# Performance work log

Measured on AMD Instinct MI355X. Metric: run time of the kernel, lower is better.

## Reference

```python
import jax, jax.numpy as jnp
import numpy as np

NW, K, C, H = 4096, 32, 256, 8
HD = C // H
POS_BND = 25            # int(0.8 * patch_size * dilation**0.5) = int(0.8*32)
RPE_NUM = 2 * POS_BND + 1  # 51; table has 3*51 = 153 rows


def setup_inputs() -> dict:
    key = jax.random.key(0)
    ks = jax.random.split(key, 10)
    s = 0.02
    return {
        "data": jax.random.normal(ks[0], (NW * K, C), jnp.float32),
        "mask": jax.random.normal(ks[1], (NW, K, K), jnp.float32),
        "rel_pos": jax.random.randint(ks[2], (NW, K, K, 3), -POS_BND, POS_BND + 1, jnp.int32),
        "qkv_w": jax.random.normal(ks[3], (C, 3 * C), jnp.float32) * s,
        "qkv_b": jnp.zeros((3 * C,), jnp.float32),
        "proj_w": jax.random.normal(ks[4], (C, C), jnp.float32) * s,
        "proj_b": jnp.zeros((C,), jnp.float32),
        "rpe_table": jax.random.normal(ks[5], (3 * RPE_NUM, H), jnp.float32) * s,
        "ln1_g": jnp.ones((C,), jnp.float32),
        "ln1_b": jnp.zeros((C,), jnp.float32),
        "ln2_g": jnp.ones((C,), jnp.float32),
        "ln2_b": jnp.zeros((C,), jnp.float32),
        "fc1_w": jax.random.normal(ks[6], (C, 4 * C), jnp.float32) * s,
        "fc1_b": jnp.zeros((4 * C,), jnp.float32),
        "fc2_w": jax.random.normal(ks[7], (4 * C, C), jnp.float32) * s,
        "fc2_b": jnp.zeros((C,), jnp.float32),
    }


def _ln(x, g, b):
    m = jnp.mean(x, axis=-1, keepdims=True)
    v = jnp.var(x, axis=-1, keepdims=True)
    return (x - m) * jax.lax.rsqrt(v + 1e-5) * g + b


def reference(data, mask, rel_pos, qkv_w, qkv_b, proj_w, proj_b, rpe_table,
              ln1_g, ln1_b, ln2_g, ln2_b, fc1_w, fc1_b, fc2_w, fc2_b):
    scale = float(HD) ** -0.5
    # pre-norm attention branch
    x = _ln(data, ln1_g, ln1_b)
    qkv = (x @ qkv_w + qkv_b).reshape(NW, K, 3, H, HD)
    q, k, v = qkv[:, :, 0], qkv[:, :, 1], qkv[:, :, 2]   # [NW,K,H,HD]
    attn = jnp.einsum('wqhd,wkhd->whqk', q * scale, k)   # [NW,H,K,K]
    # RPE: clamp xyz offsets, offset each axis into its table band, gather+sum
    idx = jnp.clip(rel_pos, -POS_BND, POS_BND) + POS_BND + jnp.arange(3) * RPE_NUM
    bias = rpe_table[idx].sum(axis=3)                    # [NW,K,K,H]
    attn = attn + bias.transpose(0, 3, 1, 2) + mask[:, None]
    attn = jax.nn.softmax(attn, axis=-1)
    out = jnp.einsum('whqk,wkhd->wqhd', attn, v).reshape(NW * K, C)
    data = data + (out @ proj_w + proj_b)
    # pre-norm MLP branch
    h = _ln(data, ln2_g, ln2_b)
    h = jax.nn.gelu(h @ fc1_w + fc1_b) @ fc2_w + fc2_b
    return data + h
```

## Files before the change

### kernel.cpp

```cpp
#include <hip/hip_runtime.h>

#define NWIN 4096
#define KTOK 32
#define CH 256
#define NH 8
#define NTOK (NWIN*KTOK)

typedef unsigned short bf16u;
typedef __attribute__((ext_vector_type(4))) float f32x4;
typedef __attribute__((ext_vector_type(4))) unsigned short u16x4;
typedef __attribute__((ext_vector_type(8))) unsigned short u16x8;
typedef __attribute__((ext_vector_type(8))) __bf16 bf16x8;

__device__ __forceinline__ unsigned short f2bf(float f) {
  unsigned u = __builtin_bit_cast(unsigned, f);
  u += 0x7fffu + ((u >> 16) & 1u);
  return (unsigned short)(u >> 16);
}

__device__ __forceinline__ f32x4 mfma16(bf16x8 a, bf16x8 b, f32x4 c) {
  return __builtin_amdgcn_mfma_f32_16x16x32_bf16(a, b, c, 0, 0, 0);
}

__device__ __forceinline__ void gl16(const void* g, void* l) {
  __builtin_amdgcn_global_load_lds(
      (const __attribute__((address_space(1))) unsigned int*)g,
      (__attribute__((address_space(3))) unsigned int*)l, 16, 0, 0);
}

__device__ __forceinline__ float gelu_f(float x) {
  float u = x + 0.044715f * x * x * x;
  return x * __builtin_amdgcn_rcpf(1.f + __expf(-1.5957691216057308f * u));
}

__global__ __launch_bounds__(256) void wprep_kernel(const float* __restrict__ W,
                                                    bf16u* __restrict__ Wt,
                                                    int Kd, int Nd) {
  int idx = blockIdx.x * 256 + threadIdx.x;
  if (idx >= Kd * Nd) return;
  int k = idx / Nd, n = idx - k * Nd;
  Wt[n * Kd + k] = f2bf(W[idx]);
}

__global__ __launch_bounds__(256) void ln_kernel(const float* __restrict__ x,
                                                 const float* __restrict__ g,
                                                 const float* __restrict__ b,
                                                 bf16u* __restrict__ y) {
  const int row = blockIdx.x * 4 + (threadIdx.x >> 6);
  const int lane = threadIdx.x & 63;
  const size_t base = (size_t)row * CH + lane * 4;
  const f32x4 v = *(const f32x4*)(x + base);
  float s = v[0] + v[1] + v[2] + v[3];
  float q = v[0]*v[0] + v[1]*v[1] + v[2]*v[2] + v[3]*v[3];
  #pragma unroll
  for (int d = 32; d; d >>= 1) { s += __shfl_xor(s, d); q += __shfl_xor(q, d); }
  const float mean = s * (1.f/256.f);
  const float rs = rsqrtf(q * (1.f/256.f) - mean*mean + 1e-5f);
  const f32x4 gv = *(const f32x4*)(g + lane*4);
  const f32x4 bv = *(const f32x4*)(b + lane*4);
  u16x4 o;
  #pragma unroll
  for (int d = 0; d < 4; ++d) o[d] = f2bf((v[d]-mean)*rs*gv[d] + bv[d]);
  *(u16x4*)(y + base) = o;
}

template<int EPI>
__global__ __launch_bounds__(256, 4)
void gemm_kernel(const bf16u* __restrict__ A, const bf16u* __restrict__ Bt,
                 const float* __restrict__ bias, const float* __restrict__ resid,
                 void* __restrict__ out, int M, int N, int K, int nx) {
  __shared__ __align__(16) char lds[32768];
  const int tid = threadIdx.x;
  const int lane = tid & 63;
  const int wv = tid >> 6;
  const int lo = lane & 15, hi = lane >> 4;
  const int nwg = gridDim.x;
  const int cpx = nwg >> 3;
  const int swz = (blockIdx.x & 7) * cpx + (blockIdx.x >> 3);
  const int by = swz / nx, bx = swz - by * nx;
  const int bm = by * 128, bn = bx * 128;
  const int wm = (wv >> 1) * 64, wn = (wv & 1) * 64;

  f32x4 acc[4][4] = {};

  const int srow = tid >> 2;
  const int sk = (tid & 3) * 16;
  const size_t rstep = (size_t)64 * K * 2;
  const char* gA = (const char*)(A + (size_t)(bm + srow) * K) + sk;
  const char* gB = (const char*)(Bt + (size_t)(bn + srow) * K) + sk;

  auto STAGE = [&](int b, int k0) {
    char* As = lds + b * 16384;
    char* Bs = As + 8192;
    const char* ga = gA + k0 * 2;
    const char* gb = gB + k0 * 2;
    gl16(ga,         As + tid*16);
    gl16(ga + rstep, As + 4096 + tid*16);
    gl16(gb,         Bs + tid*16);
    gl16(gb + rstep, Bs + 4096 + tid*16);
  };

  STAGE(0, 0);
  int cur = 0;
  for (int k0 = 0; ; k0 += 32) {
    const bool has_next = (k0 + 32 < K);
    if (has_next) {
      STAGE(cur ^ 1, k0 + 32);
      asm volatile("s_waitcnt vmcnt(4)" ::: "memory");
    } else {
      asm volatile("s_waitcnt vmcnt(0)" ::: "memory");
    }
    __builtin_amdgcn_sched_barrier(0);
    __builtin_amdgcn_s_barrier();
    const char* As = lds + cur * 16384;
    const char* Bs = As + 8192;
    bf16x8 af[4], bfv[4];
    #pragma unroll
    for (int i = 0; i < 4; ++i) {
      af[i]  = *(const bf16x8*)(As + (wm + i*16 + lo)*64 + hi*16);
      bfv[i] = *(const bf16x8*)(Bs + (wn + i*16 + lo)*64 + hi*16);
    }
    #pragma unroll
    for (int i = 0; i < 4; ++i)
      #pragma unroll
      for (int j = 0; j < 4; ++j)
        acc[i][j] = mfma16(af[i], bfv[j], acc[i][j]);
    if (!has_next) break;
    __builtin_amdgcn_s_barrier();
    cur ^= 1;
  }

  __syncthreads();
  float* Ls = (float*)(lds + wv * 4352);
  const int mb = bm + wm, nb = bn + wn;
  const int lrow = lane >> 3;
  const int lcol = (lane & 7) * 8;
  const f32x4 bv0 = *(const f32x4*)(bias + nb + lcol);
  const f32x4 bv1 = *(const f32x4*)(bias + nb + lcol + 4);

  #pragma unroll
  for (int i = 0; i < 4; ++i) {
    #pragma unroll
    for (int j = 0; j < 4; ++j)
      #pragma unroll
      for (int r = 0; r < 4; ++r)
        Ls[(hi*4 + r)*68 + j*16 + lo] = acc[i][j][r];
    #pragma unroll
    for (int p = 0; p < 2; ++p) {
      const int rr = p*8 + lrow;
      const int m = mb + i*16 + rr;
      f32x4 v0 = *(const f32x4*)(Ls + rr*68 + lcol);
      f32x4 v1 = *(const f32x4*)(Ls + rr*68 + lcol + 4);
      v0 += bv0; v1 += bv1;
      if constexpr (EPI == 2) {
        const float* rp = resid + (size_t)m*N + nb + lcol;
        v0 += *(const f32x4*)rp;
        v1 += *(const f32x4*)(rp + 4);
        float* op = (float*)out + (size_t)m*N + nb + lcol;
        *(f32x4*)op = v0;
        *(f32x4*)(op + 4) = v1;
      } else {
        if constexpr (EPI == 1) {
          #pragma unroll
          for (int d = 0; d < 4; ++d) { v0[d] = gelu_f(v0[d]); v1[d] = gelu_f(v1[d]); }
        }
        u16x8 o8;
        #pragma unroll
        for (int d = 0; d < 4; ++d) { o8[d] = f2bf(v0[d]); o8[4+d] = f2bf(v1[d]); }
        *(u16x8*)((bf16u*)out + (size_t)m*N + nb + lcol) = o8;
      }
    }
  }
}

__global__ __launch_bounds__(256, 2)
void attn_kernel(const bf16u* __restrict__ qkv, const float* __restrict__ mask,
                 const int* __restrict__ relp, const float* __restrict__ rpe,
                 bf16u* __restrict__ outp) {
  const int w = blockIdx.x;
  const int tid = threadIdx.x, lane = tid & 63, wv = tid >> 6;
  const int lo = lane & 15, hi = lane >> 4;

  __shared__ __align__(16) bf16u sQK[32*520];
  __shared__ __align__(16) bf16u sV[32][264];
  __shared__ __align__(16) bf16u sP[4][32][44];
  __shared__ float sTabT[8][156];
  __shared__ int sRel[1024];
  __shared__ float sMask[32][33];

  const size_t qbase = (size_t)w * (32*768);
  {
    #pragma unroll
    for (int t = 0; t < 8; ++t) {
      int i = tid + t*256;
      int tok = i >> 6;
      int cb = (i & 63) * 16;
      *(u16x8*)((char*)sQK + tok*1040 + cb) =
          *(const u16x8*)((const char*)(qkv + qbase) + tok*1536 + cb);
    }
    #pragma unroll
    for (int t = 0; t < 4; ++t) {
      int i = tid + t*256;
      int tok = i >> 5, c8 = i & 31;
      *(u16x8*)&sV[tok][c8*8] = *(const u16x8*)(qkv + qbase + tok*768 + 512 + c8*8);
    }
    for (int i = tid; i < 1224; i += 256)
      sTabT[i & 7][i >> 3] = rpe[i];
    #pragma unroll
    for (int t = 0; t < 4; ++t) {
      int i = tid + t*256;
      const int* rp = relp + ((size_t)w*1024 + i)*3;
      int r0 = rp[0], r1 = rp[1], r2 = rp[2];
      r0 = min(max(r0, -25), 25) + 25;
      r1 = min(max(r1, -25), 25) + 76;
      r2 = min(max(r2, -25), 25) + 127;
      sRel[i] = r0 | (r1 << 8) | (r2 << 16);
    }
    #pragma unroll
    for (int d = 0; d < 4; ++d) {
      int i = tid*4 + d;
      sMask[i >> 5][i & 31] = mask[(size_t)w*1024 + i];
    }
  }
  __syncthreads();

  const float scale = 0.17677669529663687f;
  #pragma unroll
  for (int e = 0; e < 2; ++e) {
    const int h = wv*2 + e;
    bf16x8 qf[2], kf[2];
    #pragma unroll
    for (int rf = 0; rf < 2; ++rf) {
      int tok = rf*16 + lo;
      qf[rf] = *(const bf16x8*)((const char*)sQK + tok*1040 + h*64 + hi*16);
      kf[rf] = *(const bf16x8*)((const char*)sQK + tok*1040 + 512 + h*64 + hi*16);
    }
    f32x4 S[2][2] = {};
    #pragma unroll
    for (int rf = 0; rf < 2; ++rf)
      #pragma unroll
      for (int cf = 0; cf < 2; ++cf)
        S[rf][cf] = mfma16(qf[rf], kf[cf], S[rf][cf]);
    #pragma unroll
    for (int rf = 0; rf < 2; ++rf)
      #pragma unroll
      for (int cf = 0; cf < 2; ++cf)
        #pragma unroll
        for (int r = 0; r < 4; ++r) {
          const int qq = rf*16 + hi*4 + r;
          const int kk = cf*16 + lo;
          const int pk = sRel[qq*32 + kk];
          const float bsum = sTabT[h][pk & 255] + sTabT[h][(pk >> 8) & 255]
                           + sTabT[h][(pk >> 16) & 255];
          S[rf][cf][r] = S[rf][cf][r] * scale + bsum + sMask[qq][kk];
        }
    #pragma unroll
    for (int rf = 0; rf < 2; ++rf)
      #pragma unroll
      for (int r = 0; r < 4; ++r) {
        float m0 = fmaxf(S[rf][0][r], S[rf][1][r]);
        #pragma unroll
        for (int d = 1; d < 16; d <<= 1) m0 = fmaxf(m0, __shfl_xor(m0, d));
        const float p0 = __expf(S[rf][0][r] - m0);
        const float p1 = __expf(S[rf][1][r] - m0);
        float ss = p0 + p1;
        #pragma unroll
        for (int d = 1; d < 16; d <<= 1) ss += __shfl_xor(ss, d);
        const float inv = 1.f / ss;
        S[rf][0][r] = p0 * inv;
        S[rf][1][r] = p1 * inv;
      }
    #pragma unroll
    for (int rf = 0; rf < 2; ++rf)
      #pragma unroll
      for (int cf = 0; cf < 2; ++cf)
        #pragma unroll
        for (int r = 0; r < 4; ++r)
          sP[wv][rf*16 + hi*4 + r][cf*16 + lo] = f2bf(S[rf][cf][r]);
    f32x4 O[2][2] = {};
    #pragma unroll
    for (int rf = 0; rf < 2; ++rf) {
      bf16x8 pf;
      *(u16x4*)&pf       = *(const u16x4*)&sP[wv][rf*16 + lo][hi*8];
      *((u16x4*)&pf + 1) = *(const u16x4*)&sP[wv][rf*16 + lo][hi*8 + 4];
      #pragma unroll
      for (int cf = 0; cf < 2; ++cf) {
        bf16x8 vf;
        #pragma unroll
        for (int j = 0; j < 8; ++j)
          ((bf16u*)&vf)[j] = sV[hi*8 + j][h*32 + cf*16 + lo];
        O[rf][cf] = mfma16(pf, vf, O[rf][cf]);
      }
    }
    #pragma unroll
    for (int rf = 0; rf < 2; ++rf)
      #pragma unroll
      for (int cf = 0; cf < 2; ++cf)
        #pragma unroll
        for (int r = 0; r < 4; ++r) {
          const int qq = rf*16 + hi*4 + r;
          outp[(size_t)(w*32 + qq)*256 + h*32 + cf*16 + lo] = f2bf(O[rf][cf][r]);
        }
  }
}

extern "C" void kernel_launch(void* const* d_in, const int* in_sizes, int n_in,
                              void* d_out, int out_size, void* d_ws, size_t ws_size,
                              hipStream_t stream) {
  const float* data   = (const float*)d_in[0];
  const float* mask   = (const float*)d_in[1];
  const int*   relp   = (const int*)d_in[2];
  const float* qkv_w  = (const float*)d_in[3];
  const float* qkv_b  = (const float*)d_in[4];
  const float* proj_w = (const float*)d_in[5];
  const float* proj_b = (const float*)d_in[6];
  const float* rpe    = (const float*)d_in[7];
  const float* ln1_g  = (const float*)d_in[8];
  const float* ln1_b  = (const float*)d_in[9];
  const float* ln2_g  = (const float*)d_in[10];
  const float* ln2_b  = (const float*)d_in[11];
  const float* fc1_w  = (const float*)d_in[12];
  const float* fc1_b  = (const float*)d_in[13];
  const float* fc2_w  = (const float*)d_in[14];
  const float* fc2_b  = (const float*)d_in[15];

  char* ws = (char*)d_ws;
  bf16u* wt_qkv  = (bf16u*)(ws);
  bf16u* wt_proj = (bf16u*)(ws + 393216);
  bf16u* wt_fc1  = (bf16u*)(ws + 524288);
  bf16u* wt_fc2  = (bf16u*)(ws + 1048576);
  bf16u* xbuf    = (bf16u*)(ws + 2097152);
  bf16u* qkvbuf  = (bf16u*)(ws + 2097152 + 67108864);
  float* data2   = (float*)d_out;

  wprep_kernel<<<768, 256, 0, stream>>>(qkv_w, wt_qkv, 256, 768);
  wprep_kernel<<<256, 256, 0, stream>>>(proj_w, wt_proj, 256, 256);
  wprep_kernel<<<1024, 256, 0, stream>>>(fc1_w, wt_fc1, 256, 1024);
  wprep_kernel<<<1024, 256, 0, stream>>>(fc2_w, wt_fc2, 1024, 256);

  ln_kernel<<<32768, 256, 0, stream>>>(data, ln1_g, ln1_b, xbuf);
  gemm_kernel<0><<<6*1024, 256, 0, stream>>>(xbuf, wt_qkv, qkv_b, nullptr,
                                             qkvbuf, NTOK, 768, 256, 6);
  attn_kernel<<<NWIN, 256, 0, stream>>>(qkvbuf, mask, relp, rpe, xbuf);
  gemm_kernel<2><<<2*1024, 256, 0, stream>>>(xbuf, wt_proj, proj_b, data,
                                             data2, NTOK, 256, 256, 2);
  ln_kernel<<<32768, 256, 0, stream>>>(data2, ln2_g, ln2_b, xbuf);
  gemm_kernel<1><<<8*1024, 256, 0, stream>>>(xbuf, wt_fc1, fc1_b, nullptr,
                                             qkvbuf, NTOK, 1024, 256, 8);
  gemm_kernel<2><<<2*1024, 256, 0, stream>>>(qkvbuf, wt_fc2, fc2_b, data2,
                                             d_out, NTOK, 256, 1024, 2);
}
```

Measured before the change: 623.3 us.

## Fuse LayerNorm into GEMM A-loads and triple-buffer the K-loop GEMM

LayerNorm gamma is folded into the transposed bf16 weights, and beta is folded into a precomputed bias (W^T·beta + b). That lets the QKV and FC1 GEMMs read raw fp32 activations, normalize them in registers and feed MFMA directly, so the separate LN kernels and their bf16 round trip through memory go away. A new K=256 GEMM variant keeps the whole B tile in a swizzled 64KB LDS buffer and A fragments in registers, which lowers occupancy to 2 blocks. The K=1024 GEMM moves to triple buffering with deeper prefetch at reduced occupancy.

```diff
diff --git a/kernel.cpp b/kernel.cpp
--- a/kernel.cpp
+++ b/kernel.cpp
@@ -42,34 +42,162 @@
   Wt[n * Kd + k] = f2bf(W[idx]);
 }
 
-__global__ __launch_bounds__(256) void ln_kernel(const float* __restrict__ x,
-                                                 const float* __restrict__ g,
-                                                 const float* __restrict__ b,
-                                                 bf16u* __restrict__ y) {
-  const int row = blockIdx.x * 4 + (threadIdx.x >> 6);
-  const int lane = threadIdx.x & 63;
-  const size_t base = (size_t)row * CH + lane * 4;
-  const f32x4 v = *(const f32x4*)(x + base);
-  float s = v[0] + v[1] + v[2] + v[3];
-  float q = v[0]*v[0] + v[1]*v[1] + v[2]*v[2] + v[3]*v[3];
-  #pragma unroll
-  for (int d = 32; d; d >>= 1) { s += __shfl_xor(s, d); q += __shfl_xor(q, d); }
-  const float mean = s * (1.f/256.f);
-  const float rs = rsqrtf(q * (1.f/256.f) - mean*mean + 1e-5f);
-  const f32x4 gv = *(const f32x4*)(g + lane*4);
-  const f32x4 bv = *(const f32x4*)(b + lane*4);
-  u16x4 o;
-  #pragma unroll
-  for (int d = 0; d < 4; ++d) o[d] = f2bf((v[d]-mean)*rs*gv[d] + bv[d]);
-  *(u16x4*)(y + base) = o;
+__global__ __launch_bounds__(256) void wprep_g_kernel(const float* __restrict__ W,
+                                                      const float* __restrict__ g,
+                                                      bf16u* __restrict__ Wt,
+                                                      int Kd, int Nd) {
+  int idx = blockIdx.x * 256 + threadIdx.x;
+  if (idx >= Kd * Nd) return;
+  int k = idx / Nd, n = idx - k * Nd;
+  Wt[n * Kd + k] = f2bf(W[idx] * g[k]);
+}
+
+__global__ __launch_bounds__(256) void bprep_kernel(const float* __restrict__ W,
+                                                    const float* __restrict__ bln,
+                                                    const float* __restrict__ bias,
+                                                    float* __restrict__ out,
+                                                    int Kd, int Nd) {
+  int n = blockIdx.x * 256 + threadIdx.x;
+  if (n >= Nd) return;
+  float s = bias[n];
+  for (int k = 0; k < Kd; ++k) s += bln[k] * W[(size_t)k * Nd + n];
+  out[n] = s;
+}
+
+template<int EPI, int LNA>
+__global__ __launch_bounds__(256, 2)
+void gemmB_kernel(const void* __restrict__ Av, const bf16u* __restrict__ Bt,
+                  const float* __restrict__ bias, const float* __restrict__ resid,
+                  void* __restrict__ out, int N, int nx) {
+  __shared__ __align__(16) char lds[65536];
+  const int tid = threadIdx.x, lane = tid & 63, wv = tid >> 6;
+  const int lo = lane & 15, hi = lane >> 4;
+  const int nwg = gridDim.x, cpx = nwg >> 3;
+  const int swz = (blockIdx.x & 7) * cpx + (blockIdx.x >> 3);
+  const int by = swz / nx, bx = swz - by * nx;
+  const int bm = by * 128, bn = bx * 128;
+
+  #pragma unroll
+  for (int t = 0; t < 16; ++t) {
+    const int c = t * 256 + tid;
+    const int row = c >> 5, g = c & 31;
+    gl16((const char*)Bt + (size_t)(bn + row) * 512 + ((g ^ (row & 7)) * 16),
+         lds + c * 16);
+  }
+
+  bf16x8 abf[2][8];
+  if constexpr (LNA) {
+    const float* A = (const float*)Av;
+    f32x4 av[2][8][2];
+    float sum[2] = {0, 0}, sq[2] = {0, 0};
+    #pragma unroll
+    for (int rf = 0; rf < 2; ++rf) {
+      const float* ap = A + (size_t)(bm + wv*32 + rf*16 + lo) * 256 + hi*8;
+      #pragma unroll
+      for (int j = 0; j < 8; ++j) {
+        av[rf][j][0] = *(const f32x4*)(ap + j*32);
+        av[rf][j][1] = *(const f32x4*)(ap + j*32 + 4);
+        #pragma unroll
+        for (int d = 0; d < 4; ++d) {
+          sum[rf] += av[rf][j][0][d] + av[rf][j][1][d];
+          sq[rf]  += av[rf][j][0][d]*av[rf][j][0][d] + av[rf][j][1][d]*av[rf][j][1][d];
+        }
+      }
+    }
+    #pragma unroll
+    for (int rf = 0; rf < 2; ++rf) {
+      float s = sum[rf], q = sq[rf];
+      s += __shfl_xor(s, 16); q += __shfl_xor(q, 16);
+      s += __shfl_xor(s, 32); q += __shfl_xor(q, 32);
+      const float mean = s * (1.f/256.f);
+      const float rs = rsqrtf(q * (1.f/256.f) - mean*mean + 1e-5f);
+      #pragma unroll
+      for (int j = 0; j < 8; ++j)
+        #pragma unroll
+        for (int d = 0; d < 4; ++d) {
+          ((bf16u*)&abf[rf][j])[d]     = f2bf((av[rf][j][0][d] - mean) * rs);
+          ((bf16u*)&abf[rf][j])[4 + d] = f2bf((av[rf][j][1][d] - mean) * rs);
+        }
+    }
+  } else {
+    const bf16u* A = (const bf16u*)Av;
+    #pragma unroll
+    for (int rf = 0; rf < 2; ++rf) {
+      const bf16u* ap = A + (size_t)(bm + wv*32 + rf*16 + lo) * 256 + hi*8;
+      #pragma unroll
+      for (int j = 0; j < 8; ++j)
+        abf[rf][j] = *(const bf16x8*)(ap + j*32);
+    }
+  }
+  __syncthreads();
+
+  f32x4 acc[2][8];
+  #pragma unroll
+  for (int rf = 0; rf < 2; ++rf)
+    #pragma unroll
+    for (int nf = 0; nf < 8; ++nf) acc[rf][nf] = (f32x4){0,0,0,0};
+
+  #pragma unroll
+  for (int j = 0; j < 8; ++j)
+    #pragma unroll
+    for (int nf = 0; nf < 8; ++nf) {
+      const int row = nf*16 + lo;
+      const int g = (j*4 + hi) ^ (row & 7);
+      const bf16x8 bf8 = *(const bf16x8*)(lds + row*512 + g*16);
+      acc[0][nf] = mfma16(abf[0][j], bf8, acc[0][nf]);
+      acc[1][nf] = mfma16(abf[1][j], bf8, acc[1][nf]);
+    }
+
+  __syncthreads();
+  float* Ls = (float*)(lds + wv * 8448);
+  const int ecol = (lane & 15) * 8;
+  const int erow4 = lane >> 4;
+  const f32x4 bv0 = *(const f32x4*)(bias + bn + ecol);
+  const f32x4 bv1 = *(const f32x4*)(bias + bn + ecol + 4);
+
+  #pragma unroll
+  for (int rf = 0; rf < 2; ++rf) {
+    #pragma unroll
+    for (int nf = 0; nf < 8; ++nf)
+      #pragma unroll
+      for (int r = 0; r < 4; ++r)
+        Ls[(hi*4 + r)*132 + nf*16 + lo] = acc[rf][nf][r];
+    __builtin_amdgcn_s_barrier();
+    #pragma unroll
+    for (int p = 0; p < 4; ++p) {
+      const int rr = p*4 + erow4;
+      const int m = bm + wv*32 + rf*16 + rr;
+      f32x4 v0 = *(const f32x4*)(Ls + rr*132 + ecol);
+      f32x4 v1 = *(const f32x4*)(Ls + rr*132 + ecol + 4);
+      v0 += bv0; v1 += bv1;
+      if constexpr (EPI == 2) {
+        const float* rp = resid + (size_t)m*N + bn + ecol;
+        v0 += *(const f32x4*)rp;
+        v1 += *(const f32x4*)(rp + 4);
+        float* op = (float*)out + (size_t)m*N + bn + ecol;
+        *(f32x4*)op = v0;
+        *(f32x4*)(op + 4) = v1;
+      } else {
+        if constexpr (EPI == 1) {
+          #pragma unroll
+          for (int d = 0; d < 4; ++d) { v0[d] = gelu_f(v0[d]); v1[d] = gelu_f(v1[d]); }
+        }
+        u16x8 o8;
+        #pragma unroll
+        for (int d = 0; d < 4; ++d) { o8[d] = f2bf(v0[d]); o8[4+d] = f2bf(v1[d]); }
+        *(u16x8*)((bf16u*)out + (size_t)m*N + bn + ecol) = o8;
+      }
+    }
+    if (rf == 0) __builtin_amdgcn_s_barrier();
+  }
 }
 
 template<int EPI>
-__global__ __launch_bounds__(256, 4)
+__global__ __launch_bounds__(256, 3)
 void gemm_kernel(const bf16u* __restrict__ A, const bf16u* __restrict__ Bt,
                  const float* __restrict__ bias, const float* __restrict__ resid,
                  void* __restrict__ out, int M, int N, int K, int nx) {
-  __shared__ __align__(16) char lds[32768];
+  __shared__ __align__(16) char lds[49152];
   const int tid = threadIdx.x;
   const int lane = tid & 63;
   const int wv = tid >> 6;
@@ -89,23 +217,26 @@
   const char* gA = (const char*)(A + (size_t)(bm + srow) * K) + sk;
   const char* gB = (const char*)(Bt + (size_t)(bn + srow) * K) + sk;
 
-  auto STAGE = [&](int b, int k0) {
+  auto STAGE = [&](int b, int kt) {
     char* As = lds + b * 16384;
     char* Bs = As + 8192;
-    const char* ga = gA + k0 * 2;
-    const char* gb = gB + k0 * 2;
+    const char* ga = gA + kt * 64;
+    const char* gb = gB + kt * 64;
     gl16(ga,         As + tid*16);
     gl16(ga + rstep, As + 4096 + tid*16);
     gl16(gb,         Bs + tid*16);
     gl16(gb + rstep, Bs + 4096 + tid*16);
   };
 
+  const int nt = K >> 5;
   STAGE(0, 0);
+  STAGE(1, 1);
   int cur = 0;
-  for (int k0 = 0; ; k0 += 32) {
-    const bool has_next = (k0 + 32 < K);
-    if (has_next) {
-      STAGE(cur ^ 1, k0 + 32);
+  for (int t = 0; t < nt; ++t) {
+    if (t + 2 < nt) {
+      STAGE((cur + 2) % 3, t + 2);
+      asm volatile("s_waitcnt vmcnt(8)" ::: "memory");
+    } else if (t + 1 < nt) {
       asm volatile("s_waitcnt vmcnt(4)" ::: "memory");
     } else {
       asm volatile("s_waitcnt vmcnt(0)" ::: "memory");
@@ -125,9 +256,8 @@
       #pragma unroll
       for (int j = 0; j < 4; ++j)
         acc[i][j] = mfma16(af[i], bfv[j], acc[i][j]);
-    if (!has_next) break;
     __builtin_amdgcn_s_barrier();
-    cur ^= 1;
+    cur = (cur + 1) % 3;
   }
 
   __syncthreads();
@@ -329,24 +459,26 @@
   bf16u* wt_proj = (bf16u*)(ws + 393216);
   bf16u* wt_fc1  = (bf16u*)(ws + 524288);
   bf16u* wt_fc2  = (bf16u*)(ws + 1048576);
+  float* b2_qkv  = (float*)(ws + 1572864);
+  float* b2_fc1  = (float*)(ws + 1576960);
   bf16u* xbuf    = (bf16u*)(ws + 2097152);
   bf16u* qkvbuf  = (bf16u*)(ws + 2097152 + 67108864);
   float* data2   = (float*)d_out;
 
-  wprep_kernel<<<768, 256, 0, stream>>>(qkv_w, wt_qkv, 256, 768);
+  wprep_g_kernel<<<768, 256, 0, stream>>>(qkv_w, ln1_g, wt_qkv, 256, 768);
   wprep_kernel<<<256, 256, 0, stream>>>(proj_w, wt_proj, 256, 256);
-  wprep_kernel<<<1024, 256, 0, stream>>>(fc1_w, wt_fc1, 256, 1024);
+  wprep_g_kernel<<<1024, 256, 0, stream>>>(fc1_w, ln2_g, wt_fc1, 256, 1024);
   wprep_kernel<<<1024, 256, 0, stream>>>(fc2_w, wt_fc2, 1024, 256);
-
-  ln_kernel<<<32768, 256, 0, stream>>>(data, ln1_g, ln1_b, xbuf);
-  gemm_kernel<0><<<6*1024, 256, 0, stream>>>(xbuf, wt_qkv, qkv_b, nullptr,
-                                             qkvbuf, NTOK, 768, 256, 6);
+  bprep_kernel<<<3, 256, 0, stream>>>(qkv_w, ln1_b, qkv_b, b2_qkv, 256, 768);
+  bprep_kernel<<<4, 256, 0, stream>>>(fc1_w, ln2_b, fc1_b, b2_fc1, 256, 1024);
+
+  gemmB_kernel<0,1><<<6*1024, 256, 0, stream>>>(data, wt_qkv, b2_qkv, nullptr,
+                                                qkvbuf, 768, 6);
   attn_kernel<<<NWIN, 256, 0, stream>>>(qkvbuf, mask, relp, rpe, xbuf);
-  gemm_kernel<2><<<2*1024, 256, 0, stream>>>(xbuf, wt_proj, proj_b, data,
-                                             data2, NTOK, 256, 256, 2);
-  ln_kernel<<<32768, 256, 0, stream>>>(data2, ln2_g, ln2_b, xbuf);
-  gemm_kernel<1><<<8*1024, 256, 0, stream>>>(xbuf, wt_fc1, fc1_b, nullptr,
-                                             qkvbuf, NTOK, 1024, 256, 8);
+  gemmB_kernel<2,0><<<2*1024, 256, 0, stream>>>(xbuf, wt_proj, proj_b, data,
+                                                data2, 256, 2);
+  gemmB_kernel<1,1><<<8*1024, 256, 0, stream>>>(data2, wt_fc1, b2_fc1, nullptr,
+                                                qkvbuf, 1024, 8);
   gemm_kernel<2><<<2*1024, 256, 0, stream>>>(qkvbuf, wt_fc2, fc2_b, data2,
                                              d_out, NTOK, 256, 1024, 2);
 }
```

Measured after the change: 791.6 us. 27.0% more time.

## Fuse proj GEMM with residual and LN2, triple-buffer GEMM K loop

Applied to the files above, without the earlier changes.

Adds a gemmP kernel that computes the full 256-column projection per 128-row tile, then adds bias and residual, writes data2, and applies the second LayerNorm in the epilogue. This removes the separate LN2 pass and its re-read of data2. The generic GEMM also moves from double to triple buffering with deeper vmcnt waits, to hide more load latency. In exchange, LDS use grows, occupancy drops from 4 to 3 blocks per CU, and the workspace layout changes (xnorm placed at a 256MB offset).

```diff
diff --git a/kernel.cpp b/kernel.cpp
--- a/kernel.cpp
+++ b/kernel.cpp
@@ -65,11 +65,11 @@
 }
 
 template<int EPI>
-__global__ __launch_bounds__(256, 4)
+__global__ __launch_bounds__(256, 3)
 void gemm_kernel(const bf16u* __restrict__ A, const bf16u* __restrict__ Bt,
                  const float* __restrict__ bias, const float* __restrict__ resid,
                  void* __restrict__ out, int M, int N, int K, int nx) {
-  __shared__ __align__(16) char lds[32768];
+  __shared__ __align__(16) char lds[49152];
   const int tid = threadIdx.x;
   const int lane = tid & 63;
   const int wv = tid >> 6;
@@ -89,23 +89,26 @@
   const char* gA = (const char*)(A + (size_t)(bm + srow) * K) + sk;
   const char* gB = (const char*)(Bt + (size_t)(bn + srow) * K) + sk;
 
-  auto STAGE = [&](int b, int k0) {
+  auto STAGE = [&](int b, int kt) {
     char* As = lds + b * 16384;
     char* Bs = As + 8192;
-    const char* ga = gA + k0 * 2;
-    const char* gb = gB + k0 * 2;
+    const char* ga = gA + kt * 64;
+    const char* gb = gB + kt * 64;
     gl16(ga,         As + tid*16);
     gl16(ga + rstep, As + 4096 + tid*16);
     gl16(gb,         Bs + tid*16);
     gl16(gb + rstep, Bs + 4096 + tid*16);
   };
 
+  const int nt = K >> 5;
   STAGE(0, 0);
+  STAGE(1, 1);
   int cur = 0;
-  for (int k0 = 0; ; k0 += 32) {
-    const bool has_next = (k0 + 32 < K);
-    if (has_next) {
-      STAGE(cur ^ 1, k0 + 32);
+  for (int t = 0; t < nt; ++t) {
+    if (t + 2 < nt) {
+      STAGE((cur + 2) % 3, t + 2);
+      asm volatile("s_waitcnt vmcnt(8)" ::: "memory");
+    } else if (t + 1 < nt) {
       asm volatile("s_waitcnt vmcnt(4)" ::: "memory");
     } else {
       asm volatile("s_waitcnt vmcnt(0)" ::: "memory");
@@ -125,9 +128,8 @@
       #pragma unroll
       for (int j = 0; j < 4; ++j)
         acc[i][j] = mfma16(af[i], bfv[j], acc[i][j]);
-    if (!has_next) break;
     __builtin_amdgcn_s_barrier();
-    cur ^= 1;
+    cur = (cur + 1) % 3;
   }
 
   __syncthreads();
@@ -174,6 +176,121 @@
 }
 
 __global__ __launch_bounds__(256, 2)
+void gemmP_kernel(const bf16u* __restrict__ A, const bf16u* __restrict__ Bt,
+                  const float* __restrict__ bias, const float* __restrict__ resid,
+                  float* __restrict__ out, bf16u* __restrict__ xln,
+                  const float* __restrict__ g2, const float* __restrict__ b2) {
+  __shared__ __align__(16) char lds[73728];
+  const int tid = threadIdx.x, lane = tid & 63, wv = tid >> 6;
+  const int lo = lane & 15, hi = lane >> 4;
+  const int nwg = gridDim.x, cpx = nwg >> 3;
+  const int by = (blockIdx.x & 7) * cpx + (blockIdx.x >> 3);
+  const int bm = by * 128;
+  const int wmh = wv >> 1;
+  const int wm = wmh * 64, wn = (wv & 1) * 128;
+
+  f32x4 acc[4][8] = {};
+
+  const int arow = tid >> 2;
+  const int sk = (tid & 3) * 16;
+  const char* gA = (const char*)(A + (size_t)(bm + arow) * 256) + sk;
+  const char* gB = (const char*)(Bt + (size_t)arow * 256) + sk;
+
+  auto STAGE = [&](int b, int kt) {
+    char* As = lds + b * 24576;
+    char* Bs = As + 8192;
+    const char* ga = gA + kt * 64;
+    const char* gb = gB + kt * 64;
+    gl16(ga,         As + arow*64 + sk);
+    gl16(ga + 32768, As + 4096 + arow*64 + sk);
+    #pragma unroll
+    for (int p = 0; p < 4; ++p)
+      gl16(gb + p*32768, Bs + p*4096 + arow*64 + sk);
+  };
+
+  STAGE(0, 0);
+  STAGE(1, 1);
+  int cur = 0;
+  for (int t = 0; t < 8; ++t) {
+    if (t + 2 < 8) {
+      STAGE((cur + 2) % 3, t + 2);
+      asm volatile("s_waitcnt vmcnt(12)" ::: "memory");
+    } else if (t + 1 < 8) {
+      asm volatile("s_waitcnt vmcnt(6)" ::: "memory");
+    } else {
+      asm volatile("s_waitcnt vmcnt(0)" ::: "memory");
+    }
+    __builtin_amdgcn_sched_barrier(0);
+    __builtin_amdgcn_s_barrier();
+    const char* As = lds + cur * 24576;
+    const char* Bs = As + 8192;
+    bf16x8 af[4], bf8[8];
+    #pragma unroll
+    for (int i = 0; i < 4; ++i)
+      af[i] = *(const bf16x8*)(As + (wm + i*16 + lo)*64 + hi*16);
+    #pragma unroll
+    for (int j = 0; j < 8; ++j)
+      bf8[j] = *(const bf16x8*)(Bs + (wn + j*16 + lo)*64 + hi*16);
+    #pragma unroll
+    for (int i = 0; i < 4; ++i)
+      #pragma unroll
+      for (int j = 0; j < 8; ++j)
+        acc[i][j] = mfma16(af[i], bf8[j], acc[i][j]);
+    __builtin_amdgcn_s_barrier();
+    cur = (cur + 1) % 3;
+  }
+
+  __syncthreads();
+  float* LsE = (float*)lds;
+  const int c4 = (tid & 3) * 4;
+  const int row64 = tid >> 2;
+  const int reg = row64 >> 5, rloc = row64 & 31;
+  #pragma unroll
+  for (int rr = 0; rr < 2; ++rr) {
+    #pragma unroll
+    for (int i2 = 0; i2 < 2; ++i2) {
+      const int i = rr*2 + i2;
+      #pragma unroll
+      for (int j = 0; j < 8; ++j)
+        #pragma unroll
+        for (int r = 0; r < 4; ++r)
+          LsE[wmh*8320 + (i2*16 + hi*4 + r)*260 + wn + j*16 + lo] = acc[i][j][r];
+    }
+    __syncthreads();
+    const int grow = bm + reg*64 + rr*32 + rloc;
+    f32x4 d2[16];
+    float sum = 0.f, sq = 0.f;
+    #pragma unroll
+    for (int k = 0; k < 16; ++k) {
+      const int col = c4 + k*16;
+      f32x4 v = *(const f32x4*)&LsE[reg*8320 + rloc*260 + col];
+      v += *(const f32x4*)(bias + col);
+      v += *(const f32x4*)(resid + (size_t)grow*256 + col);
+      d2[k] = v;
+      sum += v[0] + v[1] + v[2] + v[3];
+      sq  += v[0]*v[0] + v[1]*v[1] + v[2]*v[2] + v[3]*v[3];
+      *(f32x4*)(out + (size_t)grow*256 + col) = v;
+    }
+    sum += __shfl_xor(sum, 1); sq += __shfl_xor(sq, 1);
+    sum += __shfl_xor(sum, 2); sq += __shfl_xor(sq, 2);
+    const float mean = sum * (1.f/256.f);
+    const float rs = rsqrtf(sq * (1.f/256.f) - mean*mean + 1e-5f);
+    #pragma unroll
+    for (int k = 0; k < 16; ++k) {
+      const int col = c4 + k*16;
+      const f32x4 gv = *(const f32x4*)(g2 + col);
+      const f32x4 bv = *(const f32x4*)(b2 + col);
+      u16x4 o;
+      #pragma unroll
+      for (int d = 0; d < 4; ++d)
+        o[d] = f2bf((d2[k][d] - mean) * rs * gv[d] + bv[d]);
+      *(u16x4*)(xln + (size_t)grow*256 + col) = o;
+    }
+    __syncthreads();
+  }
+}
+
+__global__ __launch_bounds__(256, 2)
 void attn_kernel(const bf16u* __restrict__ qkv, const float* __restrict__ mask,
                  const int* __restrict__ relp, const float* __restrict__ rpe,
                  bf16u* __restrict__ outp) {
@@ -329,8 +446,11 @@
   bf16u* wt_proj = (bf16u*)(ws + 393216);
   bf16u* wt_fc1  = (bf16u*)(ws + 524288);
   bf16u* wt_fc2  = (bf16u*)(ws + 1048576);
-  bf16u* xbuf    = (bf16u*)(ws + 2097152);
-  bf16u* qkvbuf  = (bf16u*)(ws + 2097152 + 67108864);
+  char*  big     = ws + 2097152;
+  bf16u* xbuf    = (bf16u*)big;
+  bf16u* qkvbuf  = (bf16u*)(big + 67108864);
+  bf16u* h1      = (bf16u*)big;
+  bf16u* xnorm   = (bf16u*)(big + 268435456);
   float* data2   = (float*)d_out;
 
   wprep_kernel<<<768, 256, 0, stream>>>(qkv_w, wt_qkv, 256, 768);
@@ -338,15 +458,14 @@
   wprep_kernel<<<1024, 256, 0, stream>>>(fc1_w, wt_fc1, 256, 1024);
   wprep_kernel<<<1024, 256, 0, stream>>>(fc2_w, wt_fc2, 1024, 256);
 
-  ln_kernel<<<32768, 256, 0, stream>>>(data, ln1_g, ln1_b, xbuf);
-  gemm_kernel<0><<<6*1024, 256, 0, stream>>>(xbuf, wt_qkv, qkv_b, nullptr,
+  ln_kernel<<<32768, 256, 0, stream>>>(data, ln1_g, ln1_b, xnorm);
+  gemm_kernel<0><<<6*1024, 256, 0, stream>>>(xnorm, wt_qkv, qkv_b, nullptr,
                                              qkvbuf, NTOK, 768, 256, 6);
   attn_kernel<<<NWIN, 256, 0, stream>>>(qkvbuf, mask, relp, rpe, xbuf);
-  gemm_kernel<2><<<2*1024, 256, 0, stream>>>(xbuf, wt_proj, proj_b, data,
-                                             data2, NTOK, 256, 256, 2);
-  ln_kernel<<<32768, 256, 0, stream>>>(data2, ln2_g, ln2_b, xbuf);
-  gemm_kernel<1><<<8*1024, 256, 0, stream>>>(xbuf, wt_fc1, fc1_b, nullptr,
-                                             qkvbuf, NTOK, 1024, 256, 8);
-  gemm_kernel<2><<<2*1024, 256, 0, stream>>>(qkvbuf, wt_fc2, fc2_b, data2,
+  gemmP_kernel<<<1024, 256, 0, stream>>>(xbuf, wt_proj, proj_b, data,
+                                         data2, xnorm, ln2_g, ln2_b);
+  gemm_kernel<1><<<8*1024, 256, 0, stream>>>(xnorm, wt_fc1, fc1_b, nullptr,
+                                             h1, NTOK, 1024, 256, 8);
+  gemm_kernel<2><<<2*1024, 256, 0, stream>>>(h1, wt_fc2, fc2_b, data2,
                                              d_out, NTOK, 256, 1024, 2);
 }
```

Measured after the change: 632.7 us. About the same (+1.5%).

## Enlarge GEMM tiles to 256x256 with 512 threads and triple-buffered LDS

Applied to the files above, without the earlier changes.

Replaces the 128x128 GEMM with a 256x256 block-tile kernel: 8 waves per block, each wave computing a 128x64 sub-tile, and a three-stage LDS ring that keeps two loads in flight. The aim is more arithmetic per byte loaded and more latency hiding for the QKV, proj, fc1 and fc2 projections. The cost is a 96KB LDS footprint per block, which caps residency at one block per CU and means fewer blocks overall. The workspace layout also changes: fc1 output now sits at the start of the big buffer and the normalized activations live at a new offset 256MB in, so the kernel needs a larger workspace.

```diff
diff --git a/kernel.cpp b/kernel.cpp
--- a/kernel.cpp
+++ b/kernel.cpp
@@ -65,81 +65,83 @@
 }
 
 template<int EPI>
-__global__ __launch_bounds__(256, 4)
-void gemm_kernel(const bf16u* __restrict__ A, const bf16u* __restrict__ Bt,
-                 const float* __restrict__ bias, const float* __restrict__ resid,
-                 void* __restrict__ out, int M, int N, int K, int nx) {
-  __shared__ __align__(16) char lds[32768];
+__global__ __launch_bounds__(512, 2)
+void gemm256_kernel(const bf16u* __restrict__ A, const bf16u* __restrict__ Bt,
+                    const float* __restrict__ bias, const float* __restrict__ resid,
+                    void* __restrict__ out, int N, int K, int nx) {
+  __shared__ __align__(16) char lds[98304];
   const int tid = threadIdx.x;
   const int lane = tid & 63;
   const int wv = tid >> 6;
   const int lo = lane & 15, hi = lane >> 4;
+  const int wr = wv >> 2, wc = wv & 3;
   const int nwg = gridDim.x;
   const int cpx = nwg >> 3;
   const int swz = (blockIdx.x & 7) * cpx + (blockIdx.x >> 3);
   const int by = swz / nx, bx = swz - by * nx;
-  const int bm = by * 128, bn = bx * 128;
-  const int wm = (wv >> 1) * 64, wn = (wv & 1) * 64;
-
-  f32x4 acc[4][4] = {};
+  const int bm = by * 256, bn = bx * 256;
+
+  f32x4 acc[8][4] = {};
 
   const int srow = tid >> 2;
-  const int sk = (tid & 3) * 16;
-  const size_t rstep = (size_t)64 * K * 2;
-  const char* gA = (const char*)(A + (size_t)(bm + srow) * K) + sk;
-  const char* gB = (const char*)(Bt + (size_t)(bn + srow) * K) + sk;
-
-  auto STAGE = [&](int b, int k0) {
-    char* As = lds + b * 16384;
-    char* Bs = As + 8192;
-    const char* ga = gA + k0 * 2;
-    const char* gb = gB + k0 * 2;
-    gl16(ga,         As + tid*16);
-    gl16(ga + rstep, As + 4096 + tid*16);
-    gl16(gb,         Bs + tid*16);
-    gl16(gb + rstep, Bs + 4096 + tid*16);
+  const int sg = (tid & 3) * 16;
+  const char* pA0 = (const char*)(A + (size_t)(bm + srow) * K) + sg;
+  const char* pA1 = (const char*)(A + (size_t)(bm + 128 + srow) * K) + sg;
+  const char* pB0 = (const char*)(Bt + (size_t)(bn + srow) * K) + sg;
+  const char* pB1 = (const char*)(Bt + (size_t)(bn + 128 + srow) * K) + sg;
+
+  auto STAGE = [&](int b, int kt) {
+    char* base = lds + b * 32768;
+    const int ko = kt * 64;
+    gl16(pA0 + ko, base + tid*16);
+    gl16(pA1 + ko, base + 8192 + tid*16);
+    gl16(pB0 + ko, base + 16384 + tid*16);
+    gl16(pB1 + ko, base + 24576 + tid*16);
   };
 
+  const int nt = K >> 5;
   STAGE(0, 0);
+  STAGE(1, 1);
   int cur = 0;
-  for (int k0 = 0; ; k0 += 32) {
-    const bool has_next = (k0 + 32 < K);
-    if (has_next) {
-      STAGE(cur ^ 1, k0 + 32);
+  for (int t = 0; t < nt; ++t) {
+    if (t + 2 < nt) {
+      STAGE((cur + 2) % 3, t + 2);
+      asm volatile("s_waitcnt vmcnt(8)" ::: "memory");
+    } else if (t + 1 < nt) {
       asm volatile("s_waitcnt vmcnt(4)" ::: "memory");
     } else {
       asm volatile("s_waitcnt vmcnt(0)" ::: "memory");
     }
     __builtin_amdgcn_sched_barrier(0);
     __builtin_amdgcn_s_barrier();
-    const char* As = lds + cur * 16384;
-    const char* Bs = As + 8192;
-    bf16x8 af[4], bfv[4];
-    #pragma unroll
-    for (int i = 0; i < 4; ++i) {
-      af[i]  = *(const bf16x8*)(As + (wm + i*16 + lo)*64 + hi*16);
-      bfv[i] = *(const bf16x8*)(Bs + (wn + i*16 + lo)*64 + hi*16);
-    }
-    #pragma unroll
-    for (int i = 0; i < 4; ++i)
+    const char* As = lds + cur * 32768;
+    const char* Bs = As + 16384;
+    bf16x8 af[8], bf[4];
+    #pragma unroll
+    for (int i = 0; i < 8; ++i)
+      af[i] = *(const bf16x8*)(As + (wr*128 + i*16 + lo)*64 + hi*16);
+    #pragma unroll
+    for (int j = 0; j < 4; ++j)
+      bf[j] = *(const bf16x8*)(Bs + (wc*64 + j*16 + lo)*64 + hi*16);
+    #pragma unroll
+    for (int i = 0; i < 8; ++i)
       #pragma unroll
       for (int j = 0; j < 4; ++j)
-        acc[i][j] = mfma16(af[i], bfv[j], acc[i][j]);
-    if (!has_next) break;
+        acc[i][j] = mfma16(af[i], bf[j], acc[i][j]);
     __builtin_amdgcn_s_barrier();
-    cur ^= 1;
+    cur = (cur + 1) % 3;
   }
 
   __syncthreads();
   float* Ls = (float*)(lds + wv * 4352);
-  const int mb = bm + wm, nb = bn + wn;
+  const int mb = bm + wr*128, nb = bn + wc*64;
   const int lrow = lane >> 3;
   const int lcol = (lane & 7) * 8;
   const f32x4 bv0 = *(const f32x4*)(bias + nb + lcol);
   const f32x4 bv1 = *(const f32x4*)(bias + nb + lcol + 4);
 
   #pragma unroll
-  for (int i = 0; i < 4; ++i) {
+  for (int i = 0; i < 8; ++i) {
     #pragma unroll
     for (int j = 0; j < 4; ++j)
       #pragma unroll
@@ -329,8 +331,11 @@
   bf16u* wt_proj = (bf16u*)(ws + 393216);
   bf16u* wt_fc1  = (bf16u*)(ws + 524288);
   bf16u* wt_fc2  = (bf16u*)(ws + 1048576);
-  bf16u* xbuf    = (bf16u*)(ws + 2097152);
-  bf16u* qkvbuf  = (bf16u*)(ws + 2097152 + 67108864);
+  char*  big     = ws + 2097152;
+  bf16u* xbuf    = (bf16u*)big;
+  bf16u* qkvbuf  = (bf16u*)(big + 67108864);
+  bf16u* h1      = (bf16u*)big;
+  bf16u* xnorm   = (bf16u*)(big + 268435456);
   float* data2   = (float*)d_out;
 
   wprep_kernel<<<768, 256, 0, stream>>>(qkv_w, wt_qkv, 256, 768);
@@ -338,15 +343,15 @@
   wprep_kernel<<<1024, 256, 0, stream>>>(fc1_w, wt_fc1, 256, 1024);
   wprep_kernel<<<1024, 256, 0, stream>>>(fc2_w, wt_fc2, 1024, 256);
 
-  ln_kernel<<<32768, 256, 0, stream>>>(data, ln1_g, ln1_b, xbuf);
-  gemm_kernel<0><<<6*1024, 256, 0, stream>>>(xbuf, wt_qkv, qkv_b, nullptr,
-                                             qkvbuf, NTOK, 768, 256, 6);
+  ln_kernel<<<32768, 256, 0, stream>>>(data, ln1_g, ln1_b, xnorm);
+  gemm256_kernel<0><<<512*3, 512, 0, stream>>>(xnorm, wt_qkv, qkv_b, nullptr,
+                                               qkvbuf, 768, 256, 3);
   attn_kernel<<<NWIN, 256, 0, stream>>>(qkvbuf, mask, relp, rpe, xbuf);
-  gemm_kernel<2><<<2*1024, 256, 0, stream>>>(xbuf, wt_proj, proj_b, data,
-                                             data2, NTOK, 256, 256, 2);
-  ln_kernel<<<32768, 256, 0, stream>>>(data2, ln2_g, ln2_b, xbuf);
-  gemm_kernel<1><<<8*1024, 256, 0, stream>>>(xbuf, wt_fc1, fc1_b, nullptr,
-                                             qkvbuf, NTOK, 1024, 256, 8);
-  gemm_kernel<2><<<2*1024, 256, 0, stream>>>(qkvbuf, wt_fc2, fc2_b, data2,
-                                             d_out, NTOK, 256, 1024, 2);
-}
+  gemm256_kernel<2><<<512*1, 512, 0, stream>>>(xbuf, wt_proj, proj_b, data,
+                                               data2, 256, 256, 1);
+  ln_kernel<<<32768, 256, 0, stream>>>(data2, ln2_g, ln2_b, xnorm);
+  gemm256_kernel<1><<<512*4, 512, 0, stream>>>(xnorm, wt_fc1, fc1_b, nullptr,
+                                               h1, 1024, 256, 4);
+  gemm256_kernel<2><<<512*1, 512, 0, stream>>>(h1, wt_fc2, fc2_b, data2,
+                                               d_out, 256, 1024, 1);
+}
```

Result: slower. 641.3 us (+2.9%).
